# Optimization experiments

Hardware: AMD Instinct MI355X
Metric: run time of the kernel (lower is better)

## Reference

```python
import jax, jax.numpy as jnp
import numpy as np

# Gemma-2B style config
B, S, HID = 2, 2048, 2048
H, KH, D = 8, 1, 256          # query heads, kv heads, head_dim
THETA = 10000.0


def setup_inputs() -> dict:
    key = jax.random.key(0)
    ks = jax.random.split(key, 6)
    s = 0.02  # init scale for weights
    return {
        "hidden_states": jax.random.normal(ks[0], (B, S, HID), dtype=jnp.float32),
        "attention_mask": jnp.zeros((B, S), dtype=jnp.float32),  # additive mask over kv axis
        "position_ids": jnp.broadcast_to(jnp.arange(S, dtype=jnp.int32), (B, S)),
        "Wq": jax.random.normal(ks[1], (H * D, HID), dtype=jnp.float32) * s,
        "bq": jnp.zeros((H * D,), dtype=jnp.float32),
        "Wk": jax.random.normal(ks[2], (KH * D, HID), dtype=jnp.float32) * s,
        "bk": jnp.zeros((KH * D,), dtype=jnp.float32),
        "Wv": jax.random.normal(ks[3], (KH * D, HID), dtype=jnp.float32) * s,
        "bv": jnp.zeros((KH * D,), dtype=jnp.float32),
        "Wo": jax.random.normal(ks[4], (HID, H * D), dtype=jnp.float32) * s,
        "bo": jnp.zeros((HID,), dtype=jnp.float32),
    }


def _rope(x, position_ids):
    # x: [b, s, h, d]; rotate-half RoPE per head, computed in fp32 as in the module.
    half = D // 2
    inv_freq = 1.0 / (THETA ** (jnp.arange(0, D, 2, dtype=jnp.float32) / D))  # [d/2]
    freqs = position_ids.astype(jnp.float32)[:, :, None] * inv_freq            # [b, s, d/2]
    cos = jnp.cos(freqs)[:, :, None, :]  # [b, s, 1, d/2]
    sin = jnp.sin(freqs)[:, :, None, :]
    x1, x2 = x[..., :half], x[..., half:]
    return jnp.concatenate([cos * x1 - sin * x2, sin * x1 + cos * x2], axis=-1).astype(x.dtype)


def reference(hidden_states, attention_mask, position_ids, Wq, bq, Wk, bk, Wv, bv, Wo, bo):
    b, s, _ = hidden_states.shape
    q = (hidden_states @ Wq.T + bq).reshape(b, s, H, D)
    k = (hidden_states @ Wk.T + bk).reshape(b, s, KH, D)
    v = (hidden_states @ Wv.T + bv).reshape(b, s, KH, D)
    q = _rope(q, position_ids)
    k = _rope(k, position_ids)
    # GQA: broadcast the KV heads across query-head groups
    groups = H // KH
    k = jnp.repeat(k, groups, axis=2)  # [b, s, H, D]
    v = jnp.repeat(v, groups, axis=2)
    scores = jnp.einsum('bnhd,bmhd->bhnm', q, k) * (D ** -0.5)  # [b, H, s, s]
    scores = scores + attention_mask[:, None, None, :]
    attn = jax.nn.softmax(scores, axis=-1)  # dropout p=0.0 -> identity
    out = jnp.einsum('bhnm,bmhd->bnhd', attn, v).reshape(b, s, H * D)
    out = out @ Wo.T + bo
    return (out, attn)
```

## Files before the change

kernel.cpp:

```cpp
#include <hip/hip_runtime.h>

#define B_ 2
#define S_ 2048
#define HID_ 2048
#define H_ 8
#define D_ 256
#define NQKV 2560

typedef unsigned short u16;
typedef __attribute__((ext_vector_type(8))) short bf16x8;
typedef __attribute__((ext_vector_type(4))) float f32x4;

__device__ __forceinline__ u16 f2b(float x) {
    unsigned u = __float_as_uint(x);
    unsigned rb = (u >> 16) & 1u;
    u += 0x7fffu + rb;
    return (u16)(u >> 16);
}

__device__ __forceinline__ void load_lds16(const u16* g, u16* l) {
    __builtin_amdgcn_global_load_lds(
        (const __attribute__((address_space(1))) void*)g,
        (__attribute__((address_space(3))) void*)l, 16, 0, 0);
}

__global__ __launch_bounds__(256) void cvt_bf16(const float* __restrict__ in,
                                                u16* __restrict__ out, int n) {
    int i = (blockIdx.x * 256 + threadIdx.x) * 4;
    if (i >= n) return;
    float4 f = *(const float4*)(in + i);
    union { u16 u[4]; uint2 v; } pk;
    pk.u[0] = f2b(f.x); pk.u[1] = f2b(f.y); pk.u[2] = f2b(f.z); pk.u[3] = f2b(f.w);
    *(uint2*)(out + i) = pk.v;
}

__global__ __launch_bounds__(256) void concat_bias(const float* __restrict__ bq,
                                                   const float* __restrict__ bk,
                                                   const float* __restrict__ bv,
                                                   float* __restrict__ dst) {
    int i = blockIdx.x * 256 + threadIdx.x;
    if (i >= NQKV) return;
    float v;
    if (i < H_ * D_) v = bq[i];
    else if (i < H_ * D_ + D_) v = bk[i - H_ * D_];
    else v = bv[i - H_ * D_ - D_];
    dst[i] = v;
}

__global__ __launch_bounds__(256) void rope_kernel(const float* __restrict__ x,
                                                   int rowStride, int colOff,
                                                   const int* __restrict__ pos_ids,
                                                   u16* __restrict__ out, int nHeads) {
    int idx = blockIdx.x * 256 + threadIdx.x;
    int d   = idx & 127;
    int tmp = idx >> 7;
    int h   = tmp % nHeads;
    int n   = tmp / nHeads;
    int pos = pos_ids[n];
    float ang = (float)pos * expf(-(float)d * (9.210340371976184f / 128.0f));
    float s, c;
    sincosf(ang, &s, &c);
    size_t src = (size_t)n * rowStride + colOff + (size_t)h * D_;
    float x1 = x[src + d], x2 = x[src + d + 128];
    size_t dst = ((size_t)n * nHeads + h) * D_;
    out[dst + d]       = f2b(c * x1 - s * x2);
    out[dst + d + 128] = f2b(s * x1 + c * x2);
}

__global__ __launch_bounds__(256) void transpose_v(const float* __restrict__ v,
                                                   int rowStride, int colOff,
                                                   u16* __restrict__ vT) {
    __shared__ float t[32][33];
    int b = blockIdx.z;
    int s0 = blockIdx.x * 32, d0 = blockIdx.y * 32;
    int tx = threadIdx.x, ty = threadIdx.y;
#pragma unroll
    for (int i = 0; i < 4; ++i)
        t[ty + i * 8][tx] = v[((size_t)b * S_ + s0 + ty + i * 8) * rowStride + colOff + d0 + tx];
    __syncthreads();
#pragma unroll
    for (int i = 0; i < 4; ++i)
        vT[(size_t)b * D_ * S_ + (size_t)(d0 + ty + i * 8) * S_ + s0 + tx] = f2b(t[tx][ty + i * 8]);
}

__global__ __launch_bounds__(256) void softmax_rows(float* __restrict__ attn,
                                                    const float* __restrict__ mask,
                                                    u16* __restrict__ attn_b) {
    int row = blockIdx.x;
    int b = row >> 14;
    float* p = attn + (size_t)row * S_;
    const float* mb = mask + (size_t)b * S_;
    int t = threadIdx.x;
    const float sc = 0.0625f;

    float4 v0 = *(float4*)(p + t * 4);
    float4 v1 = *(float4*)(p + 1024 + t * 4);
    float4 m0 = *(const float4*)(mb + t * 4);
    float4 m1 = *(const float4*)(mb + 1024 + t * 4);
    float x[8] = { v0.x * sc + m0.x, v0.y * sc + m0.y, v0.z * sc + m0.z, v0.w * sc + m0.w,
                   v1.x * sc + m1.x, v1.y * sc + m1.y, v1.z * sc + m1.z, v1.w * sc + m1.w };

    float mx = x[0];
#pragma unroll
    for (int j = 1; j < 8; ++j) mx = fmaxf(mx, x[j]);
#pragma unroll
    for (int o = 32; o > 0; o >>= 1) mx = fmaxf(mx, __shfl_down(mx, o));
    __shared__ float redm[4], reds[4];
    int lane = t & 63, w = t >> 6;
    if (lane == 0) redm[w] = mx;
    __syncthreads();
    mx = fmaxf(fmaxf(redm[0], redm[1]), fmaxf(redm[2], redm[3]));

    float e[8], s = 0.f;
#pragma unroll
    for (int j = 0; j < 8; ++j) { e[j] = expf(x[j] - mx); s += e[j]; }
#pragma unroll
    for (int o = 32; o > 0; o >>= 1) s += __shfl_down(s, o);
    if (lane == 0) reds[w] = s;
    __syncthreads();
    s = reds[0] + reds[1] + reds[2] + reds[3];
    float inv = 1.f / s;

    float o8[8];
#pragma unroll
    for (int j = 0; j < 8; ++j) o8[j] = e[j] * inv;
    *(float4*)(p + t * 4)        = make_float4(o8[0], o8[1], o8[2], o8[3]);
    *(float4*)(p + 1024 + t * 4) = make_float4(o8[4], o8[5], o8[6], o8[7]);

    if (attn_b) {
        u16* pb = attn_b + (size_t)row * S_;
        union { u16 u[4]; uint2 v; } k0, k1;
#pragma unroll
        for (int j = 0; j < 4; ++j) { k0.u[j] = f2b(o8[j]); k1.u[j] = f2b(o8[4 + j]); }
        *(uint2*)(pb + t * 4)        = k0.v;
        *(uint2*)(pb + 1024 + t * 4) = k1.v;
    }
}

#define TILE_M 128
#define TILE_N 128
#define TILE_K 32

template <bool C_IS_BF16>
__global__ __launch_bounds__(256, 2) void gemm_async(
    const u16* __restrict__ Ap, const u16* __restrict__ Bp, void* __restrict__ Cp,
    const float* __restrict__ bias, int lda, int ldb, int ldc, int K,
    long sAb, long sAh, long sBb, long sBh, long sCb, long sCh, int numH) {
    __shared__ __align__(16) u16 As[TILE_M * TILE_K];
    __shared__ __align__(16) u16 Bs[TILE_N * TILE_K];

    int z = blockIdx.z;
    int bb = z / numH, hh = z % numH;
    const u16* Ab = Ap + (long)bb * sAb + (long)hh * sAh;
    const u16* Bb = Bp + (long)bb * sBb + (long)hh * sBh;
    long cOff = (long)bb * sCb + (long)hh * sCh;

    const int m0 = blockIdx.y * TILE_M;
    const int n0 = blockIdx.x * TILE_N;
    const int tid = threadIdx.x;
    const int lane = tid & 63, wave = tid >> 6;
    const int l15 = lane & 15, quad = lane >> 4;
    const int waveM = wave >> 1, waveN = wave & 1;

    f32x4 acc[4][4];
#pragma unroll
    for (int mt = 0; mt < 4; ++mt)
#pragma unroll
        for (int nt = 0; nt < 4; ++nt)
#pragma unroll
            for (int r = 0; r < 4; ++r) acc[mt][nt][r] = 0.f;

    int rowS[2], colS[2];
    u16 *lA[2], *lB[2];
#pragma unroll
    for (int i = 0; i < 2; ++i) {
        int c = i * 256 + tid;
        rowS[i] = c >> 2;
        colS[i] = (((c & 3) ^ ((rowS[i] >> 1) & 3)) * 8);
        lA[i] = As + (size_t)(i * 256 + wave * 64) * 8;
        lB[i] = Bs + (size_t)(i * 256 + wave * 64) * 8;
    }

    for (int k0 = 0; k0 < K; k0 += TILE_K) {
#pragma unroll
        for (int i = 0; i < 2; ++i) {
            load_lds16(Ab + (size_t)(m0 + rowS[i]) * lda + k0 + colS[i], lA[i]);
            load_lds16(Bb + (size_t)(n0 + rowS[i]) * ldb + k0 + colS[i], lB[i]);
        }
        __syncthreads();

        bf16x8 av[4], bv[4];
#pragma unroll
        for (int t = 0; t < 4; ++t) {
            int ra = waveM * 64 + t * 16 + l15;
            av[t] = *(bf16x8*)&As[ra * TILE_K + ((quad ^ ((ra >> 1) & 3)) * 8)];
            int rb = waveN * 64 + t * 16 + l15;
            bv[t] = *(bf16x8*)&Bs[rb * TILE_K + ((quad ^ ((rb >> 1) & 3)) * 8)];
        }
#pragma unroll
        for (int mt = 0; mt < 4; ++mt)
#pragma unroll
            for (int nt = 0; nt < 4; ++nt)
                acc[mt][nt] = __builtin_amdgcn_mfma_f32_16x16x32_bf16(av[mt], bv[nt],
                                                                      acc[mt][nt], 0, 0, 0);
        __syncthreads();
    }

#pragma unroll
    for (int mt = 0; mt < 4; ++mt) {
        int row = m0 + waveM * 64 + mt * 16 + quad * 4;
#pragma unroll
        for (int nt = 0; nt < 4; ++nt) {
            int col = n0 + waveN * 64 + nt * 16 + l15;
            float bia = bias ? bias[col] : 0.f;
#pragma unroll
            for (int r = 0; r < 4; ++r) {
                float val = acc[mt][nt][r] + bia;
                if constexpr (C_IS_BF16)
                    ((u16*)Cp)[cOff + (size_t)(row + r) * ldc + col] = f2b(val);
                else
                    ((float*)Cp)[cOff + (size_t)(row + r) * ldc + col] = val;
            }
        }
    }
}

#define LDSK 40
__global__ __launch_bounds__(256, 2) void gemm_slow_f32a(
    const float* __restrict__ Ap, const u16* __restrict__ Bp, u16* __restrict__ Cp,
    int lda, int ldb, int ldc, int K,
    long sAb, long sAh, long sBb, long sBh, long sCb, long sCh, int numH) {
    __shared__ __align__(16) u16 As[TILE_M * LDSK];
    __shared__ __align__(16) u16 Bs[TILE_N * LDSK];
    int z = blockIdx.z;
    int bb = z / numH, hh = z % numH;
    const float* Af = Ap + (long)bb * sAb + (long)hh * sAh;
    const u16* Bb = Bp + (long)bb * sBb + (long)hh * sBh;
    long cOff = (long)bb * sCb + (long)hh * sCh;
    const int m0 = blockIdx.y * TILE_M, n0 = blockIdx.x * TILE_N;
    const int tid = threadIdx.x;
    const int lane = tid & 63, wave = tid >> 6;
    const int l15 = lane & 15, quad = lane >> 4;
    const int waveM = wave >> 1, waveN = wave & 1;
    f32x4 acc[4][4];
#pragma unroll
    for (int mt = 0; mt < 4; ++mt)
#pragma unroll
        for (int nt = 0; nt < 4; ++nt)
#pragma unroll
            for (int r = 0; r < 4; ++r) acc[mt][nt][r] = 0.f;
    for (int k0 = 0; k0 < K; k0 += TILE_K) {
#pragma unroll
        for (int i = 0; i < 2; ++i) {
            int c = tid + i * 256;
            int row = c >> 2, col = (c & 3) * 8;
            const float* src = Af + (size_t)(m0 + row) * lda + k0 + col;
            float4 f0 = *(const float4*)src;
            float4 f1 = *(const float4*)(src + 4);
            union { u16 u[8]; uint4 v; } pk;
            pk.u[0] = f2b(f0.x); pk.u[1] = f2b(f0.y); pk.u[2] = f2b(f0.z); pk.u[3] = f2b(f0.w);
            pk.u[4] = f2b(f1.x); pk.u[5] = f2b(f1.y); pk.u[6] = f2b(f1.z); pk.u[7] = f2b(f1.w);
            *(uint4*)&As[row * LDSK + col] = pk.v;
            *(uint4*)&Bs[row * LDSK + col] =
                *(const uint4*)(Bb + (size_t)(n0 + row) * ldb + k0 + col);
        }
        __syncthreads();
        bf16x8 av[4], bv[4];
#pragma unroll
        for (int t = 0; t < 4; ++t) {
            av[t] = *(bf16x8*)&As[(waveM * 64 + t * 16 + l15) * LDSK + quad * 8];
            bv[t] = *(bf16x8*)&Bs[(waveN * 64 + t * 16 + l15) * LDSK + quad * 8];
        }
#pragma unroll
        for (int mt = 0; mt < 4; ++mt)
#pragma unroll
            for (int nt = 0; nt < 4; ++nt)
                acc[mt][nt] = __builtin_amdgcn_mfma_f32_16x16x32_bf16(av[mt], bv[nt],
                                                                      acc[mt][nt], 0, 0, 0);
        __syncthreads();
    }
#pragma unroll
    for (int mt = 0; mt < 4; ++mt) {
        int row = m0 + waveM * 64 + mt * 16 + quad * 4;
#pragma unroll
        for (int nt = 0; nt < 4; ++nt) {
            int col = n0 + waveN * 64 + nt * 16 + l15;
#pragma unroll
            for (int r = 0; r < 4; ++r)
                Cp[cOff + (size_t)(row + r) * ldc + col] = f2b(acc[mt][nt][r]);
        }
    }
}

extern "C" void kernel_launch(void* const* d_in, const int* in_sizes, int n_in,
                              void* d_out, int out_size, void* d_ws, size_t ws_size,
                              hipStream_t stream) {
    const float* hs   = (const float*)d_in[0];
    const float* mask = (const float*)d_in[1];
    const int*   pos  = (const int*)d_in[2];
    const float* Wq = (const float*)d_in[3];
    const float* bq = (const float*)d_in[4];
    const float* Wk = (const float*)d_in[5];
    const float* bk = (const float*)d_in[6];
    const float* Wv = (const float*)d_in[7];
    const float* bv = (const float*)d_in[8];
    const float* Wo = (const float*)d_in[9];
    const float* bo = (const float*)d_in[10];

    float* out  = (float*)d_out;
    float* attn = (float*)d_out + (size_t)B_ * S_ * HID_;

    char* ws = (char*)d_ws;
    size_t need = 0;
    u16* hs_b    = (u16*)(ws);          need += (size_t)B_ * S_ * HID_ * 2;
    u16* Wqkv_b  = (u16*)(ws + need);   need += (size_t)NQKV * HID_ * 2;
    u16* Wo_b    = (u16*)(ws + need);   need += (size_t)HID_ * H_ * D_ * 2;
    float* qkv_f = (float*)(ws + need); need += (size_t)B_ * S_ * NQKV * 4;
    u16* q_b     = (u16*)(ws + need);   need += (size_t)B_ * S_ * H_ * D_ * 2;
    u16* k_b     = (u16*)(ws + need);   need += (size_t)B_ * S_ * D_ * 2;
    u16* vT_b    = (u16*)(ws + need);   need += (size_t)B_ * D_ * S_ * 2;
    float* bqkv  = (float*)(ws + need); need += (size_t)NQKV * 4 + 4096;
    need &= ~(size_t)255;
    u16* attn_b  = (u16*)(ws + need);
    size_t need_big = need + (size_t)B_ * H_ * S_ * S_ * 2;
    bool big = ws_size >= need_big;
    u16* ctx_b = hs_b;

    cvt_bf16<<<dim3((B_ * S_ * HID_) / 1024), 256, 0, stream>>>(hs, hs_b, B_ * S_ * HID_);
    cvt_bf16<<<dim3((H_ * D_ * HID_) / 1024), 256, 0, stream>>>(Wq, Wqkv_b, H_ * D_ * HID_);
    cvt_bf16<<<dim3((D_ * HID_) / 1024), 256, 0, stream>>>(Wk, Wqkv_b + (size_t)H_ * D_ * HID_, D_ * HID_);
    cvt_bf16<<<dim3((D_ * HID_) / 1024), 256, 0, stream>>>(Wv, Wqkv_b + (size_t)(H_ * D_ + D_) * HID_, D_ * HID_);
    cvt_bf16<<<dim3((HID_ * H_ * D_) / 1024), 256, 0, stream>>>(Wo, Wo_b, HID_ * H_ * D_);
    concat_bias<<<dim3((NQKV + 255) / 256), 256, 0, stream>>>(bq, bk, bv, bqkv);

    gemm_async<false><<<dim3(NQKV / TILE_N, (B_ * S_) / TILE_M, 1), 256, 0, stream>>>(
        hs_b, Wqkv_b, qkv_f, bqkv, HID_, HID_, NQKV, HID_,
        0, 0, 0, 0, 0, 0, 1);

    rope_kernel<<<dim3((B_ * S_ * H_ * 128) / 256), 256, 0, stream>>>(
        qkv_f, NQKV, 0, pos, q_b, H_);
    rope_kernel<<<dim3((B_ * S_ * 1 * 128) / 256), 256, 0, stream>>>(
        qkv_f, NQKV, H_ * D_, pos, k_b, 1);
    transpose_v<<<dim3(S_ / 32, D_ / 32, B_), dim3(32, 8), 0, stream>>>(
        qkv_f, NQKV, H_ * D_ + D_, vT_b);

    gemm_async<false><<<dim3(S_ / TILE_N, S_ / TILE_M, B_ * H_), 256, 0, stream>>>(
        q_b, k_b, attn, nullptr, H_ * D_, D_, S_, D_,
        (long)S_ * H_ * D_, D_,
        (long)S_ * D_, 0,
        (long)H_ * S_ * S_, (long)S_ * S_,
        H_);

    softmax_rows<<<dim3(B_ * H_ * S_), 256, 0, stream>>>(attn, mask, big ? attn_b : nullptr);

    if (big) {
        gemm_async<true><<<dim3(D_ / TILE_N, S_ / TILE_M, B_ * H_), 256, 0, stream>>>(
            attn_b, vT_b, ctx_b, nullptr, S_, S_, H_ * D_, S_,
            (long)H_ * S_ * S_, (long)S_ * S_,
            (long)D_ * S_, 0,
            (long)S_ * H_ * D_, D_,
            H_);
    } else {
        gemm_slow_f32a<<<dim3(D_ / TILE_N, S_ / TILE_M, B_ * H_), 256, 0, stream>>>(
            attn, vT_b, ctx_b, S_, S_, H_ * D_, S_,
            (long)H_ * S_ * S_, (long)S_ * S_,
            (long)D_ * S_, 0,
            (long)S_ * H_ * D_, D_,
            H_);
    }

    gemm_async<false><<<dim3(HID_ / TILE_N, (B_ * S_) / TILE_M, 1), 256, 0, stream>>>(
        ctx_b, Wo_b, out, bo, H_ * D_, H_ * D_, HID_, H_ * D_,
        0, 0, 0, 0, 0, 0, 1);
}
```

Baseline: 760.0 us.

## Fuse QK^T score GEMM with row softmax in a single kernel

```diff
diff --git a/kernel.cpp b/kernel.cpp
--- a/kernel.cpp
+++ b/kernel.cpp
@@ -83,57 +83,128 @@
         vT[(size_t)b * D_ * S_ + (size_t)(d0 + ty + i * 8) * S_ + s0 + tx] = f2b(t[tx][ty + i * 8]);
 }
 
-__global__ __launch_bounds__(256) void softmax_rows(float* __restrict__ attn,
-                                                    const float* __restrict__ mask,
-                                                    u16* __restrict__ attn_b) {
-    int row = blockIdx.x;
-    int b = row >> 14;
-    float* p = attn + (size_t)row * S_;
-    const float* mb = mask + (size_t)b * S_;
-    int t = threadIdx.x;
+__global__ __launch_bounds__(512, 2) void score_softmax(
+    const u16* __restrict__ q_b, const u16* __restrict__ k_b,
+    const float* __restrict__ mask, float* __restrict__ attn,
+    u16* __restrict__ attn_b) {
+    __shared__ __align__(16) u16 qs[32 * 256];
+    __shared__ float redm[8][16], reds[8][16];
+
+    const int z = blockIdx.z;
+    const int bb = z >> 3, hh = z & 7;
+    const int n0 = blockIdx.x * 32;
+    const int tid = threadIdx.x;
+    const int lane = tid & 63, wave = tid >> 6;
+    const int l15 = lane & 15, quad = lane >> 4;
+    const int rg = wave >> 2, cg = wave & 3;
+
+    const u16* qsrc = q_b + (((size_t)bb * S_ + n0) * H_ + hh) * D_;
+#pragma unroll
+    for (int i = 0; i < 2; ++i) {
+        int c = i * 512 + tid;
+        int row = c >> 5, sg = c & 31;
+        int g = sg ^ (row & 7);
+        load_lds16(qsrc + (size_t)row * (H_ * D_) + g * 8,
+                   qs + (size_t)(i * 512 + wave * 64) * 8);
+    }
+
+    f32x4 acc[32];
+#pragma unroll
+    for (int ct = 0; ct < 32; ++ct)
+#pragma unroll
+        for (int r = 0; r < 4; ++r) acc[ct][r] = 0.f;
+
+    __syncthreads();
+
+    bf16x8 av[8];
+    const int rr = rg * 16 + l15;
+#pragma unroll
+    for (int kk = 0; kk < 8; ++kk)
+        av[kk] = *(const bf16x8*)&qs[rr * 256 + (((kk * 4 + quad) ^ (rr & 7)) * 8)];
+
+    const u16* kb = k_b + (size_t)bb * S_ * D_ + (size_t)(cg * 512 + l15) * D_ + quad * 8;
+#pragma unroll
+    for (int ct = 0; ct < 32; ++ct) {
+        const u16* kr = kb + (size_t)ct * 16 * D_;
+        bf16x8 bv[8];
+#pragma unroll
+        for (int kk = 0; kk < 8; ++kk) bv[kk] = *(const bf16x8*)(kr + kk * 32);
+#pragma unroll
+        for (int kk = 0; kk < 8; ++kk)
+            acc[ct] = __builtin_amdgcn_mfma_f32_16x16x32_bf16(av[kk], bv[kk], acc[ct], 0, 0, 0);
+    }
+
     const float sc = 0.0625f;
-
-    float4 v0 = *(float4*)(p + t * 4);
-    float4 v1 = *(float4*)(p + 1024 + t * 4);
-    float4 m0 = *(const float4*)(mb + t * 4);
-    float4 m1 = *(const float4*)(mb + 1024 + t * 4);
-    float x[8] = { v0.x * sc + m0.x, v0.y * sc + m0.y, v0.z * sc + m0.z, v0.w * sc + m0.w,
-                   v1.x * sc + m1.x, v1.y * sc + m1.y, v1.z * sc + m1.z, v1.w * sc + m1.w };
-
-    float mx = x[0];
-#pragma unroll
-    for (int j = 1; j < 8; ++j) mx = fmaxf(mx, x[j]);
-#pragma unroll
-    for (int o = 32; o > 0; o >>= 1) mx = fmaxf(mx, __shfl_down(mx, o));
-    __shared__ float redm[4], reds[4];
-    int lane = t & 63, w = t >> 6;
-    if (lane == 0) redm[w] = mx;
+    const float* maskb = mask + (size_t)bb * S_ + cg * 512 + l15;
+    float mx[4] = {-3.4e38f, -3.4e38f, -3.4e38f, -3.4e38f};
+#pragma unroll
+    for (int ct = 0; ct < 32; ++ct) {
+        float mkv = maskb[ct * 16];
+#pragma unroll
+        for (int r = 0; r < 4; ++r) {
+            float xv = acc[ct][r] * sc + mkv;
+            acc[ct][r] = xv;
+            mx[r] = fmaxf(mx[r], xv);
+        }
+    }
+#pragma unroll
+    for (int off = 1; off < 16; off <<= 1)
+#pragma unroll
+        for (int r = 0; r < 4; ++r) mx[r] = fmaxf(mx[r], __shfl_xor(mx[r], off));
+    if (l15 == 0) {
+#pragma unroll
+        for (int r = 0; r < 4; ++r) redm[wave][quad * 4 + r] = mx[r];
+    }
     __syncthreads();
-    mx = fmaxf(fmaxf(redm[0], redm[1]), fmaxf(redm[2], redm[3]));
-
-    float e[8], s = 0.f;
-#pragma unroll
-    for (int j = 0; j < 8; ++j) { e[j] = expf(x[j] - mx); s += e[j]; }
-#pragma unroll
-    for (int o = 32; o > 0; o >>= 1) s += __shfl_down(s, o);
-    if (lane == 0) reds[w] = s;
+    float fm[4], sm[4];
+#pragma unroll
+    for (int r = 0; r < 4; ++r) {
+        int rw = quad * 4 + r;
+        fm[r] = fmaxf(fmaxf(redm[rg * 4 + 0][rw], redm[rg * 4 + 1][rw]),
+                      fmaxf(redm[rg * 4 + 2][rw], redm[rg * 4 + 3][rw]));
+        sm[r] = 0.f;
+    }
+#pragma unroll
+    for (int ct = 0; ct < 32; ++ct)
+#pragma unroll
+        for (int r = 0; r < 4; ++r) {
+            float e = expf(acc[ct][r] - fm[r]);
+            acc[ct][r] = e;
+            sm[r] += e;
+        }
+#pragma unroll
+    for (int off = 1; off < 16; off <<= 1)
+#pragma unroll
+        for (int r = 0; r < 4; ++r) sm[r] += __shfl_xor(sm[r], off);
+    if (l15 == 0) {
+#pragma unroll
+        for (int r = 0; r < 4; ++r) reds[wave][quad * 4 + r] = sm[r];
+    }
     __syncthreads();
-    s = reds[0] + reds[1] + reds[2] + reds[3];
-    float inv = 1.f / s;
-
-    float o8[8];
-#pragma unroll
-    for (int j = 0; j < 8; ++j) o8[j] = e[j] * inv;
-    *(float4*)(p + t * 4)        = make_float4(o8[0], o8[1], o8[2], o8[3]);
-    *(float4*)(p + 1024 + t * 4) = make_float4(o8[4], o8[5], o8[6], o8[7]);
-
+
+    size_t obase = ((size_t)(bb * H_ + hh) * S_ + n0 + rg * 16 + quad * 4) * S_
+                 + cg * 512 + l15;
+#pragma unroll
+    for (int r = 0; r < 4; ++r) {
+        int rw = quad * 4 + r;
+        float inv = 1.f / (reds[rg * 4 + 0][rw] + reds[rg * 4 + 1][rw] +
+                           reds[rg * 4 + 2][rw] + reds[rg * 4 + 3][rw]);
+        float* ao = attn + obase + (size_t)r * S_;
+#pragma unroll
+        for (int ct = 0; ct < 32; ++ct) {
+            float p = acc[ct][r] * inv;
+            ao[ct * 16] = p;
+            acc[ct][r] = p;
+        }
+    }
     if (attn_b) {
-        u16* pb = attn_b + (size_t)row * S_;
-        union { u16 u[4]; uint2 v; } k0, k1;
-#pragma unroll
-        for (int j = 0; j < 4; ++j) { k0.u[j] = f2b(o8[j]); k1.u[j] = f2b(o8[4 + j]); }
-        *(uint2*)(pb + t * 4)        = k0.v;
-        *(uint2*)(pb + 1024 + t * 4) = k1.v;
+        u16* ab = attn_b + obase;
+#pragma unroll
+        for (int r = 0; r < 4; ++r) {
+            u16* abr = ab + (size_t)r * S_;
+#pragma unroll
+            for (int ct = 0; ct < 32; ++ct) abr[ct * 16] = f2b(acc[ct][r]);
+        }
     }
 }
 
@@ -344,14 +415,8 @@
     transpose_v<<<dim3(S_ / 32, D_ / 32, B_), dim3(32, 8), 0, stream>>>(
         qkv_f, NQKV, H_ * D_ + D_, vT_b);
 
-    gemm_async<false><<<dim3(S_ / TILE_N, S_ / TILE_M, B_ * H_), 256, 0, stream>>>(
-        q_b, k_b, attn, nullptr, H_ * D_, D_, S_, D_,
-        (long)S_ * H_ * D_, D_,
-        (long)S_ * D_, 0,
-        (long)H_ * S_ * S_, (long)S_ * S_,
-        H_);
-
-    softmax_rows<<<dim3(B_ * H_ * S_), 256, 0, stream>>>(attn, mask, big ? attn_b : nullptr);
+    score_softmax<<<dim3(S_ / 32, 1, B_ * H_), 512, 0, stream>>>(
+        q_b, k_b, mask, attn, big ? attn_b : nullptr);
 
     if (big) {
         gemm_async<true><<<dim3(D_ / TILE_N, S_ / TILE_M, B_ * H_), 256, 0, stream>>>(
```

New measurement: 857.0 us. 12.8% more time.
